# Performance work log

Hardware: AMD Instinct MI355X
Metric: run time of the kernel (lower is better)

The kernel has to match this reference:

```python
import jax, jax.numpy as jnp
import numpy as np

B, T, DM, H, DH = 4, 2048, 1024, 16, 64
DI = H * DH
CLIP = 1.0
LN_EPS = 1e-5


def setup_inputs() -> dict:
    key = jax.random.key(0)
    ks = jax.random.split(key, 9)

    def xav(k, shape):  # xavier_uniform, fan_in=shape[1], fan_out=shape[0]
        lim = float(np.sqrt(6.0 / (shape[0] + shape[1])))
        return jax.random.uniform(k, shape, jnp.float32, -lim, lim)

    def kai(k, shape):  # default nn.Linear weight init
        lim = float(1.0 / np.sqrt(shape[1]))
        return jax.random.uniform(k, shape, jnp.float32, -lim, lim)

    return {
        "x": jax.random.normal(ks[0], (B, T, DM), jnp.float32),
        "Wq": xav(ks[1], (DI, DM)),
        "Wk": xav(ks[2], (DI, DM)),
        "Wv": xav(ks[3], (DI, DM)),
        "Wa": kai(ks[4], (DI, DM)), "ba": jnp.full((DI,), 3.0, jnp.float32),
        "Wb": kai(ks[5], (H, DM)), "bb": jnp.zeros((H,), jnp.float32),
        "Wg": kai(ks[6], (H, DM)), "bg": jnp.zeros((H,), jnp.float32),
        "WaR": kai(ks[7], (DI, DM)), "baR": jnp.full((DI,), 3.0, jnp.float32),
        "Wo": xav(ks[8], (DM, DI)),
        "ln_w": jnp.ones((DM,), jnp.float32),
        "ln_b": jnp.zeros((DM,), jnp.float32),
    }


def reference(x, Wq, Wk, Wv, Wa, ba, Wb, bb, Wg, bg, WaR, baR, Wo, ln_w, ln_b):
    Bs, Ts, _ = x.shape
    residual = x
    # LayerNorm
    mu = jnp.mean(x, -1, keepdims=True)
    var = jnp.mean((x - mu) ** 2, -1, keepdims=True)
    xn = (x - mu) / jnp.sqrt(var + LN_EPS) * ln_w + ln_b

    q = (xn @ Wq.T).reshape(Bs, Ts, H, DH)
    k = (xn @ Wk.T).reshape(Bs, Ts, H, DH)
    v = (xn @ Wv.T).reshape(Bs, Ts, H, DH)
    alpha = jax.nn.sigmoid(xn @ Wa.T + ba).reshape(Bs, Ts, H, DH)
    aR = jax.nn.sigmoid(xn @ WaR.T + baR).reshape(Bs, Ts, H, DH)
    beta = jax.nn.sigmoid(xn @ Wb.T + bb)   # (B,T,H)
    gamma = jax.nn.sigmoid(xn @ Wg.T + bg)  # (B,T,H)

    tm = lambda a: jnp.moveaxis(a, 1, 0)  # time-major for scan
    xs = (tm(q), tm(k), tm(v), tm(alpha), tm(aR), tm(beta), tm(gamma))
    S0 = jnp.zeros((Bs, H, DH, DH), x.dtype)

    def step(carry, inp):
        S, R = carry
        q_t, k_t, v_t, a_t, aR_t, b_t, g_t = inp  # (B,H,d) / (B,H)
        kn = k_t / jnp.maximum(jnp.linalg.norm(k_t, axis=-1, keepdims=True), 1e-12)
        # residual target from previous state: r = clip(v - S^T k)
        pred = jnp.einsum('bhji,bhj->bhi', S, kn)
        r = jnp.clip(v_t - pred, -CLIP, CLIP)
        # primary state: S = diag(alpha) S; S += beta k (v - k^T S)
        S = a_t[..., None] * S
        kp = jnp.einsum('bhd,bhde->bhe', kn, S)
        S = S + b_t[..., None, None] * kn[..., None] * (v_t - kp)[..., None, :]
        o = jnp.einsum('bhji,bhj->bhi', S, q_t)
        # residual state
        R = aR_t[..., None] * R
        kpR = jnp.einsum('bhd,bhde->bhe', kn, R)
        R = R + g_t[..., None, None] * kn[..., None] * (r - kpR)[..., None, :]
        o = o + jnp.einsum('bhji,bhj->bhi', R, q_t)
        return (S, R), o

    _, os = jax.lax.scan(step, (S0, S0), xs)  # os: (T,B,H,d)
    out = jnp.moveaxis(os, 0, 1).reshape(Bs, Ts, DI) @ Wo.T
    return out + residual  # dropout is identity at inference
```

## Files before the change

kernel.cpp:

```cpp
#include <hip/hip_runtime.h>
#include <hip/hip_fp16.h>

#define B_SZ 4
#define T_SEQ 2048
#define NH 16
#define HD 64
#define DMODEL 1024
#define MTOT (B_SZ * T_SEQ)

typedef __bf16 bf16x8 __attribute__((ext_vector_type(8)));
typedef float f32x4 __attribute__((ext_vector_type(4)));
typedef float f32x2 __attribute__((ext_vector_type(2)));
typedef _Float16 f16x4 __attribute__((ext_vector_type(4)));

__device__ __forceinline__ unsigned short f2bf(float f) {
    union { float f; unsigned int i; } c; c.f = f;
    unsigned int u = c.i;
    u += 0x7fffu + ((u >> 16) & 1u);
    return (unsigned short)(u >> 16);
}
__device__ __forceinline__ float sigm(float x) { return 1.f / (1.f + __expf(-x)); }

__device__ __forceinline__ void dma16(const void* g, void* l) {
    __builtin_amdgcn_global_load_lds(
        (const __attribute__((address_space(1))) void*)g,
        (__attribute__((address_space(3))) void*)l, 16, 0, 0);
}

template <int CTRL>
__device__ __forceinline__ float dppadd(float x) {
    int v = __builtin_amdgcn_update_dpp(0, __builtin_bit_cast(int, x), CTRL, 0xf, 0xf, false);
    return x + __builtin_bit_cast(float, v);
}
__device__ __forceinline__ float rowsum16(float x) {
    x = dppadd<0x128>(x);
    x = dppadd<0x124>(x);
    x = dppadd<0x122>(x);
    x = dppadd<0x121>(x);
    return x;
}

__device__ __forceinline__ void rowsum3(float& a, float& b, float& c) {
    a = rowsum16(a);
    b = rowsum16(b);
    c = rowsum16(c);
}

__global__ __launch_bounds__(256, 1) void k_ln(const float* __restrict__ x,
                                               const float* __restrict__ lnw,
                                               const float* __restrict__ lnb,
                                               unsigned short* __restrict__ xn) {
    const int m = blockIdx.x;
    const int t = threadIdx.x;
    float4 xv = ((const float4*)(x + (size_t)m * DMODEL))[t];
    float s = xv.x + xv.y + xv.z + xv.w;
    float s2 = xv.x * xv.x + xv.y * xv.y + xv.z * xv.z + xv.w * xv.w;
#pragma unroll
    for (int off = 32; off >= 1; off >>= 1) {
        s += __shfl_xor(s, off);
        s2 += __shfl_xor(s2, off);
    }
    __shared__ float red[8];
    const int wid = t >> 6;
    if ((t & 63) == 0) { red[wid] = s; red[4 + wid] = s2; }
    __syncthreads();
    if (t == 0) {
        float su = red[0] + red[1] + red[2] + red[3];
        float sq = red[4] + red[5] + red[6] + red[7];
        float mu = su * (1.f / DMODEL);
        float var = sq * (1.f / DMODEL) - mu * mu;
        red[0] = mu;
        red[1] = rsqrtf(var + 1e-5f);
    }
    __syncthreads();
    float mu = red[0], rstd = red[1];
    float4 w4 = ((const float4*)lnw)[t];
    float4 b4 = ((const float4*)lnb)[t];
    ushort4 o;
    o.x = f2bf((xv.x - mu) * rstd * w4.x + b4.x);
    o.y = f2bf((xv.y - mu) * rstd * w4.y + b4.y);
    o.z = f2bf((xv.z - mu) * rstd * w4.z + b4.z);
    o.w = f2bf((xv.w - mu) * rstd * w4.w + b4.w);
    ((ushort4*)(xn + (size_t)m * DMODEL))[t] = o;
}

struct WPtrs { const float* p0; const float* p1; const float* p2; const float* p3; const float* p4; };

__global__ __launch_bounds__(256, 1) void k_wconv(WPtrs w, unsigned short* __restrict__ dst) {
    const int plane = blockIdx.y;
    const float* src = plane == 0 ? w.p0 : plane == 1 ? w.p1 : plane == 2 ? w.p2
                                                             : plane == 3 ? w.p3 : w.p4;
    const size_t i = ((size_t)blockIdx.x * 256 + threadIdx.x) * 8;
    float4 f0 = *(const float4*)(src + i);
    float4 f1 = *(const float4*)(src + i + 4);
    uint4 o;
    o.x = (unsigned)f2bf(f0.x) | ((unsigned)f2bf(f0.y) << 16);
    o.y = (unsigned)f2bf(f0.z) | ((unsigned)f2bf(f0.w) << 16);
    o.z = (unsigned)f2bf(f1.x) | ((unsigned)f2bf(f1.y) << 16);
    o.w = (unsigned)f2bf(f1.z) | ((unsigned)f2bf(f1.w) << 16);
    *(uint4*)(dst + (size_t)plane * 1048576 + i) = o;
}

__global__ __launch_bounds__(256, 1) void k_cvt1(const float* __restrict__ src,
                                                 unsigned short* __restrict__ dst) {
    const size_t i = ((size_t)blockIdx.x * 256 + threadIdx.x) * 8;
    float4 f0 = *(const float4*)(src + i);
    float4 f1 = *(const float4*)(src + i + 4);
    uint4 o;
    o.x = (unsigned)f2bf(f0.x) | ((unsigned)f2bf(f0.y) << 16);
    o.y = (unsigned)f2bf(f0.z) | ((unsigned)f2bf(f0.w) << 16);
    o.z = (unsigned)f2bf(f1.x) | ((unsigned)f2bf(f1.y) << 16);
    o.w = (unsigned)f2bf(f1.z) | ((unsigned)f2bf(f1.w) << 16);
    *(uint4*)(dst + i) = o;
}

template <int KDIM>
__device__ __forceinline__ void gemm128(const unsigned short* __restrict__ A,
                                        const unsigned short* __restrict__ Bw,
                                        int m0, int n0, f32x4 acc[4][4]) {
    __shared__ __align__(16) unsigned short sA[128 * 32];
    __shared__ __align__(16) unsigned short sB[128 * 32];

    const int t = threadIdx.x;
    const int lane = t & 63;
    const int wv = t >> 6;
    const int wm = wv >> 1, wn = wv & 1;
    const int ml = lane & 15, kq = lane >> 4;

#pragma unroll
    for (int i = 0; i < 4; i++)
#pragma unroll
        for (int j = 0; j < 4; j++) {
            f32x4 z; z[0] = 0.f; z[1] = 0.f; z[2] = 0.f; z[3] = 0.f;
            acc[i][j] = z;
        }

    const unsigned short* pA = A + (size_t)m0 * KDIM;
    const unsigned short* pB = Bw + (size_t)n0 * KDIM;
    const unsigned short* gA0 = pA + (size_t)(t >> 2) * KDIM + (t & 3) * 8;
    const unsigned short* gA1 = gA0 + (size_t)64 * KDIM;
    const unsigned short* gB0 = pB + (size_t)(t >> 2) * KDIM + (t & 3) * 8;
    const unsigned short* gB1 = gB0 + (size_t)64 * KDIM;
    unsigned short* lA0 = sA + wv * 512;
    unsigned short* lA1 = lA0 + 2048;
    unsigned short* lB0 = sB + wv * 512;
    unsigned short* lB1 = lB0 + 2048;

    for (int kb = 0; kb < KDIM / 32; kb++) {
        const int ko = kb * 32;
        dma16(gA0 + ko, lA0);
        dma16(gA1 + ko, lA1);
        dma16(gB0 + ko, lB0);
        dma16(gB1 + ko, lB1);
        __syncthreads();
        bf16x8 af[4], bfr[4];
#pragma unroll
        for (int mt = 0; mt < 4; mt++)
            af[mt] = *(const bf16x8*)&sA[(wm * 64 + mt * 16 + ml) * 32 + kq * 8];
#pragma unroll
        for (int nt = 0; nt < 4; nt++)
            bfr[nt] = *(const bf16x8*)&sB[(wn * 64 + nt * 16 + ml) * 32 + kq * 8];
#pragma unroll
        for (int mt = 0; mt < 4; mt++)
#pragma unroll
            for (int nt = 0; nt < 4; nt++)
                acc[mt][nt] = __builtin_amdgcn_mfma_f32_16x16x32_bf16(af[mt], bfr[nt], acc[mt][nt], 0, 0, 0);
        __syncthreads();
    }
}

template <typename OT>
__global__ __launch_bounds__(256, 1) void k_proj(const unsigned short* __restrict__ xn,
                                                 const unsigned short* __restrict__ wbf,
                                                 const float* __restrict__ ba,
                                                 const float* __restrict__ baR,
                                                 OT* __restrict__ qo, OT* __restrict__ ko,
                                                 OT* __restrict__ vo, OT* __restrict__ ao,
                                                 OT* __restrict__ aRo) {
    const int m0 = blockIdx.x * 128;
    const int yt = blockIdx.y;
    const int widx = yt >> 3;
    const int n0 = (yt & 7) * 128;
    const unsigned short* W = wbf + (size_t)widx * 1048576;
    f32x4 acc[4][4];
    gemm128<1024>(xn, W, m0, n0, acc);

    OT* outp = widx == 0 ? qo : widx == 1 ? ko : widx == 2 ? vo : widx == 3 ? ao : aRo;
    const float* bias = (widx == 3) ? ba : (widx == 4) ? baR : (const float*)0;
    const int lane = threadIdx.x & 63;
    const int wv = threadIdx.x >> 6;
    const int wm = wv >> 1, wn = wv & 1;
    const int ml = lane & 15, kq = lane >> 4;
#pragma unroll
    for (int mt = 0; mt < 4; mt++)
#pragma unroll
        for (int nt = 0; nt < 4; nt++) {
            const int rowg = m0 + wm * 64 + mt * 16 + kq * 4;
            const int colg = n0 + wn * 64 + nt * 16 + ml;
            float bval = bias ? bias[colg] : 0.f;
#pragma unroll
            for (int r = 0; r < 4; r++) {
                float v = acc[mt][nt][r];
                if (widx >= 3) v = sigm(v + bval);
                outp[(size_t)(rowg + r) * DMODEL + colg] = (OT)v;
            }
        }
}

__global__ __launch_bounds__(256, 1) void k_bg(const unsigned short* __restrict__ xn,
                                               const float* __restrict__ Wb,
                                               const float* __restrict__ bb,
                                               const float* __restrict__ Wg,
                                               const float* __restrict__ bgp,
                                               f32x2* __restrict__ bgpk) {
    const int m = blockIdx.x;
    const int t = threadIdx.x;
    const int h = t >> 4, seg = t & 15;
    const ushort4* xr = (const ushort4*)(xn + (size_t)m * DMODEL + seg * 64);
    const float4* wbr = (const float4*)(Wb + (size_t)h * DMODEL + seg * 64);
    const float4* wgr = (const float4*)(Wg + (size_t)h * DMODEL + seg * 64);
    float db = 0.f, dg = 0.f;
#pragma unroll
    for (int u = 0; u < 16; u++) {
        ushort4 a = xr[u];
        float4 w1 = wbr[u], w2 = wgr[u];
        union { unsigned int i; float f; } c0, c1, c2, c3;
        c0.i = ((unsigned int)a.x) << 16; c1.i = ((unsigned int)a.y) << 16;
        c2.i = ((unsigned int)a.z) << 16; c3.i = ((unsigned int)a.w) << 16;
        db += c0.f * w1.x + c1.f * w1.y + c2.f * w1.z + c3.f * w1.w;
        dg += c0.f * w2.x + c1.f * w2.y + c2.f * w2.z + c3.f * w2.w;
    }
#pragma unroll
    for (int off = 1; off < 16; off <<= 1) {
        db += __shfl_xor(db, off);
        dg += __shfl_xor(dg, off);
    }
    if (seg == 0) {
        f32x2 o;
        o[0] = sigm(db + bb[h]);
        o[1] = sigm(dg + bgp[h]);
        bgpk[(size_t)m * NH + h] = o;
    }
}

__global__ __launch_bounds__(256, 1) void k_prep16(__half* __restrict__ kb) {
    const int row = blockIdx.x * 16 + (threadIdx.x >> 4);
    const int tr = threadIdx.x & 15;
    const int bh = row >> 11, t = row & 2047;
    const size_t idx = ((size_t)((bh >> 4) * T_SEQ + t)) * DMODEL + (bh & 15) * 64 + tr * 4;
    f16x4 k4 = *(const f16x4*)((const __half*)kb + idx);
    float k0 = (float)k4[0], k1 = (float)k4[1], k2 = (float)k4[2], k3 = (float)k4[3];
    float ss = k0 * k0 + k1 * k1 + k2 * k2 + k3 * k3;
    ss = rowsum16(ss);
    float inv = 1.f / fmaxf(sqrtf(ss), 1e-12f);
    f16x4 o;
    o[0] = (_Float16)(k0 * inv); o[1] = (_Float16)(k1 * inv);
    o[2] = (_Float16)(k2 * inv); o[3] = (_Float16)(k3 * inv);
    *(f16x4*)(kb + idx) = o;
}

__global__ __launch_bounds__(256, 1) void k_prep32(float* __restrict__ kb) {
    const int row = blockIdx.x * 16 + (threadIdx.x >> 4);
    const int tr = threadIdx.x & 15;
    const int bh = row >> 11, t = row & 2047;
    const size_t idx = ((size_t)((bh >> 4) * T_SEQ + t)) * DMODEL + (bh & 15) * 64 + tr * 4;
    f32x4 k4 = *(const f32x4*)(kb + idx);
    float ss = k4[0] * k4[0] + k4[1] * k4[1] + k4[2] * k4[2] + k4[3] * k4[3];
    ss = rowsum16(ss);
    float inv = 1.f / fmaxf(sqrtf(ss), 1e-12f);
    f32x4 o;
    o[0] = k4[0] * inv; o[1] = k4[1] * inv; o[2] = k4[2] * inv; o[3] = k4[3] * inv;
    *(f32x4*)(kb + idx) = o;
}

__global__ __launch_bounds__(256, 1) void k_scan32(const float* __restrict__ qb,
                                                   const float* __restrict__ knb,
                                                   const float* __restrict__ vb,
                                                   const float* __restrict__ ab,
                                                   const float* __restrict__ aRb,
                                                   const f32x2* __restrict__ bgpk,
                                                   unsigned short* __restrict__ ob) {
    const int blk = blockIdx.x;
    const int bh = blk & 63, cg = blk >> 6;
    const int b = bh >> 4, h = bh & 15;
    const int t = threadIdx.x;
    const int col = t >> 4, tr = t & 15;
    const int ii = cg * 16 + col;
    const int j0 = tr * 4;

    const size_t blkoff = (size_t)b * T_SEQ * DMODEL + h * 64;
    const float* pq = qb + blkoff;
    const float* pk = knb + blkoff;
    const float* pa = ab + blkoff;
    const float* pr = aRb + blkoff;
    const float* pvb = vb + blkoff;
    const f32x2* pbg = bgpk + (size_t)b * T_SEQ * NH + h;
    unsigned short* obp = ob + blkoff + ii;

    f32x2 S01 = {0.f, 0.f}, S23 = {0.f, 0.f}, R01 = {0.f, 0.f}, R23 = {0.f, 0.f};

    f32x4 rk[6], rq[6], ra[6], rr[6];
    float rv[6];
    f32x2 rbg[6];

#pragma unroll
    for (int p = 0; p < 6; p++) {
        const size_t vo = (size_t)p * DMODEL;
        rk[p] = *(const f32x4*)(pk + vo + j0);
        rq[p] = *(const f32x4*)(pq + vo + j0);
        ra[p] = *(const f32x4*)(pa + vo + j0);
        rr[p] = *(const f32x4*)(pr + vo + j0);
        rv[p] = pvb[vo + ii];
        rbg[p] = pbg[(size_t)p * NH];
    }

    float oA, oB, oC;

#define SCAN_BODY32(P, ODEST)                                                       \
    {                                                                               \
        const f32x2 kn01 = {rk[P][0], rk[P][1]}, kn23 = {rk[P][2], rk[P][3]};       \
        const f32x2 a01 = {ra[P][0], ra[P][1]}, a23 = {ra[P][2], ra[P][3]};         \
        const f32x2 x01 = {rr[P][0], rr[P][1]}, x23 = {rr[P][2], rr[P][3]};         \
        const f32x2 q01 = {rq[P][0], rq[P][1]}, q23 = {rq[P][2], rq[P][3]};         \
        const float vc = rv[P];                                                     \
        const float beta = rbg[P][0], gamma = rbg[P][1];                            \
        const f32x2 Sd01 = a01 * S01, Sd23 = a23 * S23;                             \
        const f32x2 Rd01 = x01 * R01, Rd23 = x23 * R23;                             \
        const f32x2 pv2 = S01 * kn01 + S23 * kn23;                                  \
        const f32x2 kp2 = Sd01 * kn01 + Sd23 * kn23;                                \
        const f32x2 kR2 = Rd01 * kn01 + Rd23 * kn23;                                \
        float pred = pv2[0] + pv2[1];                                               \
        float kp = kp2[0] + kp2[1];                                                 \
        float kpR = kR2[0] + kR2[1];                                                \
        rowsum3(pred, kp, kpR);                                                     \
        const float rres = fminf(fmaxf(vc - pred, -1.f), 1.f);                      \
        const float cS = beta * (vc - kp);                                          \
        const float cR = gamma * (rres - kpR);                                      \
        const f32x2 cS2 = {cS, cS}, cR2 = {cR, cR};                                 \
        S01 = cS2 * kn01 + Sd01; S23 = cS2 * kn23 + Sd23;                           \
        R01 = cR2 * kn01 + Rd01; R23 = cR2 * kn23 + Rd23;                           \
        const f32x2 ov = (S01 + R01) * q01 + (S23 + R23) * q23;                     \
        ODEST = ov[0] + ov[1];                                                      \
              \
        {                                                                           \
            const int sp = (st + (P) + 6) & (T_SEQ - 1);                            \
            const size_t vo = (size_t)sp * DMODEL;                                  \
            rk[P] = *(const f32x4*)(pk + vo + j0);                                  \
            rq[P] = *(const f32x4*)(pq + vo + j0);                                  \
            ra[P] = *(const f32x4*)(pa + vo + j0);                                  \
            rr[P] = *(const f32x4*)(pr + vo + j0);                                  \
            rv[P] = pvb[vo + ii];                                                   \
            rbg[P] = pbg[(size_t)sp * NH];                                          \
        }                                                                           \
    }

#define FLUSH3(SBASE)                                                               \
    {                                                                               \
        rowsum3(oA, oB, oC);                                                        \
        if (tr == 0) {                                                              \
            if ((SBASE) < T_SEQ)     obp[(size_t)(SBASE) * DMODEL] = f2bf(oA);      \
            if ((SBASE) + 1 < T_SEQ) obp[(size_t)((SBASE) + 1) * DMODEL] = f2bf(oB);\
            if ((SBASE) + 2 < T_SEQ) obp[(size_t)((SBASE) + 2) * DMODEL] = f2bf(oC);\
        }                                                                           \
    }

    for (int st = 0; st < T_SEQ; st += 6) {
        SCAN_BODY32(0, oA)
        SCAN_BODY32(1, oB)
        SCAN_BODY32(2, oC)
        FLUSH3(st)
        SCAN_BODY32(3, oA)
        SCAN_BODY32(4, oB)
        SCAN_BODY32(5, oC)
        FLUSH3(st + 3)
    }
#undef SCAN_BODY32
#undef FLUSH3
}

__global__ __launch_bounds__(256, 1) void k_scan16(const __half* __restrict__ qb,
                                                   const __half* __restrict__ knb,
                                                   const __half* __restrict__ vb,
                                                   const __half* __restrict__ ab,
                                                   const __half* __restrict__ aRb,
                                                   const f32x2* __restrict__ bgpk,
                                                   unsigned short* __restrict__ ob) {
    const int blk = blockIdx.x;
    const int bh = blk & 63, cg = blk >> 6;
    const int b = bh >> 4, h = bh & 15;
    const int t = threadIdx.x;
    const int col = t >> 4, tr = t & 15;
    const int ii = cg * 16 + col;
    const int j0 = tr * 4;

    const size_t vecbase = ((size_t)b * T_SEQ) * DMODEL + h * 64 + j0;
    const size_t vbase = ((size_t)b * T_SEQ) * DMODEL + h * 64 + ii;
    const size_t bgbase = ((size_t)b * T_SEQ) * NH + h;

    const __half* pk = knb + vecbase;
    const __half* pq = qb + vecbase;
    const __half* pa = ab + vecbase;
    const __half* pr = aRb + vecbase;

    float S0 = 0, S1 = 0, S2 = 0, S3 = 0, R0 = 0, R1 = 0, R2 = 0, R3 = 0;

    f16x4 rk[6], rq[6], ra[6], rr[6];
    __half rv[6];
    f32x2 rbg[6];
    f32x4 fkn[6], fq[6], fa[6], fr[6];
    float fv[6];

#pragma unroll
    for (int p = 0; p < 6; p++) {
        const size_t voff = (size_t)p * DMODEL;
        rk[p] = *(const f16x4*)(pk + voff);
        rq[p] = *(const f16x4*)(pq + voff);
        ra[p] = *(const f16x4*)(pa + voff);
        rr[p] = *(const f16x4*)(pr + voff);
        rv[p] = vb[vbase + voff];
        rbg[p] = bgpk[bgbase + (size_t)p * NH];
    }
    fkn[0][0] = (float)rk[0][0]; fkn[0][1] = (float)rk[0][1]; fkn[0][2] = (float)rk[0][2]; fkn[0][3] = (float)rk[0][3];
    fq[0][0] = (float)rq[0][0]; fq[0][1] = (float)rq[0][1]; fq[0][2] = (float)rq[0][2]; fq[0][3] = (float)rq[0][3];
    fa[0][0] = (float)ra[0][0]; fa[0][1] = (float)ra[0][1]; fa[0][2] = (float)ra[0][2]; fa[0][3] = (float)ra[0][3];
    fr[0][0] = (float)rr[0][0]; fr[0][1] = (float)rr[0][1]; fr[0][2] = (float)rr[0][2]; fr[0][3] = (float)rr[0][3];
    fv[0] = (float)rv[0];

#define SCAN_BODY(P, PN)                                                              \
    {                                                                                 \
        const int s = st + (P);                                                       \
        const float beta = rbg[P][0], gamma = rbg[P][1];                              \
        {                                                                             \
            const size_t voff = (size_t)((s + 6) & (T_SEQ - 1)) * DMODEL;             \
            rk[P] = *(const f16x4*)(pk + voff);                                       \
            rq[P] = *(const f16x4*)(pq + voff);                                       \
            ra[P] = *(const f16x4*)(pa + voff);                                       \
            rr[P] = *(const f16x4*)(pr + voff);                                       \
            rv[P] = vb[vbase + voff];                                                 \
        }                                                                             \
        fkn[PN][0] = (float)rk[PN][0]; fkn[PN][1] = (float)rk[PN][1];                 \
        fkn[PN][2] = (float)rk[PN][2]; fkn[PN][3] = (float)rk[PN][3];                 \
        fq[PN][0] = (float)rq[PN][0]; fq[PN][1] = (float)rq[PN][1];                   \
        fq[PN][2] = (float)rq[PN][2]; fq[PN][3] = (float)rq[PN][3];                   \
        fa[PN][0] = (float)ra[PN][0]; fa[PN][1] = (float)ra[PN][1];                   \
        fa[PN][2] = (float)ra[PN][2]; fa[PN][3] = (float)ra[PN][3];                   \
        fr[PN][0] = (float)rr[PN][0]; fr[PN][1] = (float)rr[PN][1];                   \
        fr[PN][2] = (float)rr[PN][2]; fr[PN][3] = (float)rr[PN][3];                   \
        fv[PN] = (float)rv[PN];                                                       \
        {                                                                             \
            const float kn0 = fkn[P][0], kn1 = fkn[P][1], kn2 = fkn[P][2], kn3 = fkn[P][3]; \
            const float a0 = fa[P][0], a1 = fa[P][1], a2 = fa[P][2], a3 = fa[P][3];   \
            const float x0 = fr[P][0], x1 = fr[P][1], x2 = fr[P][2], x3 = fr[P][3];   \
            const float vc = fv[P];                                                   \
            float pred = S0 * kn0 + S1 * kn1 + S2 * kn2 + S3 * kn3;                   \
            float Sd0 = a0 * S0, Sd1 = a1 * S1, Sd2 = a2 * S2, Sd3 = a3 * S3;         \
            float Rd0 = x0 * R0, Rd1 = x1 * R1, Rd2 = x2 * R2, Rd3 = x3 * R3;         \
            float kp = Sd0 * kn0 + Sd1 * kn1 + Sd2 * kn2 + Sd3 * kn3;                 \
            float kpR = Rd0 * kn0 + Rd1 * kn1 + Rd2 * kn2 + Rd3 * kn3;                \
            pred = rowsum16(pred);                                                    \
            kp = rowsum16(kp);                                                        \
            kpR = rowsum16(kpR);                                                      \
            const float rres = fminf(fmaxf(vc - pred, -1.f), 1.f);                    \
            const float cS = beta * (vc - kp);                                        \
            const float cR = gamma * (rres - kpR);                                    \
            S0 = fmaf(cS, kn0, Sd0); S1 = fmaf(cS, kn1, Sd1);                         \
            S2 = fmaf(cS, kn2, Sd2); S3 = fmaf(cS, kn3, Sd3);                         \
            R0 = fmaf(cR, kn0, Rd0); R1 = fmaf(cR, kn1, Rd1);                         \
            R2 = fmaf(cR, kn2, Rd2); R3 = fmaf(cR, kn3, Rd3);                         \
            float o = (S0 + R0) * fq[P][0] + (S1 + R1) * fq[P][1] +                   \
                      (S2 + R2) * fq[P][2] + (S3 + R3) * fq[P][3];                    \
            o = rowsum16(o);                                                          \
            if (tr == 0 && s < T_SEQ)                                                 \
                ob[vbase + (size_t)s * DMODEL] = f2bf(o);                             \
        }                                                                             \
        rbg[P] = bgpk[bgbase + (size_t)((s + 6) & (T_SEQ - 1)) * NH];                 \
    }

    for (int st = 0; st < T_SEQ; st += 6) {
        SCAN_BODY(0, 1)
        SCAN_BODY(1, 2)
        SCAN_BODY(2, 3)
        SCAN_BODY(3, 4)
        SCAN_BODY(4, 5)
        SCAN_BODY(5, 0)
    }
#undef SCAN_BODY
}

__global__ __launch_bounds__(256, 1) void k_out(const unsigned short* __restrict__ ob,
                                                const unsigned short* __restrict__ wobf,
                                                const float* __restrict__ x,
                                                float* __restrict__ out) {
    const int m0 = blockIdx.x * 128;
    const int n0 = blockIdx.y * 128;
    f32x4 acc[4][4];
    gemm128<1024>(ob, wobf, m0, n0, acc);
    const int lane = threadIdx.x & 63;
    const int wv = threadIdx.x >> 6;
    const int wm = wv >> 1, wn = wv & 1;
    const int ml = lane & 15, kq = lane >> 4;
#pragma unroll
    for (int mt = 0; mt < 4; mt++)
#pragma unroll
        for (int nt = 0; nt < 4; nt++) {
            const int rowg = m0 + wm * 64 + mt * 16 + kq * 4;
            const int colg = n0 + wn * 64 + nt * 16 + ml;
#pragma unroll
            for (int r = 0; r < 4; r++) {
                size_t idx = (size_t)(rowg + r) * DMODEL + colg;
                out[idx] = acc[mt][nt][r] + x[idx];
            }
        }
}

extern "C" void kernel_launch(void* const* d_in, const int* in_sizes, int n_in,
                              void* d_out, int out_size, void* d_ws, size_t ws_size,
                              hipStream_t stream) {
    const float* x = (const float*)d_in[0];
    const float* Wq = (const float*)d_in[1];
    const float* Wk = (const float*)d_in[2];
    const float* Wv = (const float*)d_in[3];
    const float* Wa = (const float*)d_in[4];
    const float* ba = (const float*)d_in[5];
    const float* Wb = (const float*)d_in[6];
    const float* bb = (const float*)d_in[7];
    const float* Wg = (const float*)d_in[8];
    const float* bg = (const float*)d_in[9];
    const float* WaR = (const float*)d_in[10];
    const float* baR = (const float*)d_in[11];
    const float* Wo = (const float*)d_in[12];
    const float* lnw = (const float*)d_in[13];
    const float* lnb = (const float*)d_in[14];

    const size_t SZH = 16777216ULL;
    const size_t SZF = 33554432ULL;
    const size_t need32 = 5 * SZF + SZH + 2097152ULL;
    const size_t need16 = 6 * SZH + 2097152ULL;

    char* ws = (char*)d_ws;
    unsigned short* wbf = (unsigned short*)d_out;
    WPtrs wp{Wq, Wk, Wv, Wa, WaR};

    if (ws_size >= need32) {
        float* qb = (float*)(ws + 0 * SZF);
        float* kb = (float*)(ws + 1 * SZF);
        float* vb = (float*)(ws + 2 * SZF);
        float* ab = (float*)(ws + 3 * SZF);
        float* aRb = (float*)(ws + 4 * SZF);
        unsigned short* xn = (unsigned short*)(ws + 5 * SZF);
        f32x2* bgpk = (f32x2*)(ws + 5 * SZF + SZH);
        unsigned short* wobf = (unsigned short*)qb;

        k_wconv<<<dim3(512, 5), dim3(256), 0, stream>>>(wp, wbf);
        k_ln<<<dim3(MTOT), dim3(256), 0, stream>>>(x, lnw, lnb, xn);
        k_proj<float><<<dim3(64, 40), dim3(256), 0, stream>>>(xn, wbf, ba, baR, qb, kb, vb, ab, aRb);
        k_bg<<<dim3(MTOT), dim3(256), 0, stream>>>(xn, Wb, bb, Wg, bg, bgpk);
        k_prep32<<<dim3(MTOT * NH / 16), dim3(256), 0, stream>>>(kb);
        k_scan32<<<dim3(256), dim3(256), 0, stream>>>(qb, kb, vb, ab, aRb, bgpk, xn);
        k_cvt1<<<dim3(512), dim3(256), 0, stream>>>(Wo, wobf);
        k_out<<<dim3(64, 8), dim3(256), 0, stream>>>(xn, wobf, x, (float*)d_out);
    } else if (ws_size >= need16) {
        __half* qb = (__half*)(ws + 0 * SZH);
        __half* kb = (__half*)(ws + 1 * SZH);
        __half* vb = (__half*)(ws + 2 * SZH);
        __half* ab = (__half*)(ws + 3 * SZH);
        __half* aRb = (__half*)(ws + 4 * SZH);
        unsigned short* xn = (unsigned short*)(ws + 5 * SZH);
        f32x2* bgpk = (f32x2*)(ws + 6 * SZH);
        unsigned short* wobf = (unsigned short*)qb;

        k_wconv<<<dim3(512, 5), dim3(256), 0, stream>>>(wp, wbf);
        k_ln<<<dim3(MTOT), dim3(256), 0, stream>>>(x, lnw, lnb, xn);
        k_proj<_Float16><<<dim3(64, 40), dim3(256), 0, stream>>>(
            xn, wbf, ba, baR, (_Float16*)qb, (_Float16*)kb, (_Float16*)vb, (_Float16*)ab, (_Float16*)aRb);
        k_bg<<<dim3(MTOT), dim3(256), 0, stream>>>(xn, Wb, bb, Wg, bg, bgpk);
        k_prep16<<<dim3(MTOT * NH / 16), dim3(256), 0, stream>>>(kb);
        k_scan16<<<dim3(256), dim3(256), 0, stream>>>(qb, kb, vb, ab, aRb, bgpk, xn);
        k_cvt1<<<dim3(512), dim3(256), 0, stream>>>(Wo, wobf);
        k_out<<<dim3(64, 8), dim3(256), 0, stream>>>(xn, wobf, x, (float*)d_out);
    }
}
```

Before: 835.5 us.

## Split scan state columns across 32 lanes and double scan block count

The recurrent scan kernel now gives each state column 32 lanes holding 2 elements each, instead of 16 lanes holding 4, and launches 512 blocks instead of 256 with launch bounds allowing two blocks per CU. This shortens the per-lane serial arithmetic on the critical recurrence path and raises occupancy on the latency-bound scan. The cost is an extra cross-row shuffle in every reduction and more redundant per-block loads of k, q, alpha and aR.

```diff
diff --git a/kernel.cpp b/kernel.cpp
--- a/kernel.cpp
+++ b/kernel.cpp
@@ -41,6 +41,15 @@
 }
 
 __device__ __forceinline__ void rowsum3(float& a, float& b, float& c) {
+    a = rowsum16(a);
+    b = rowsum16(b);
+    c = rowsum16(c);
+}
+
+__device__ __forceinline__ void rowsum32_3(float& a, float& b, float& c) {
+    a += __shfl_xor(a, 16);
+    b += __shfl_xor(b, 16);
+    c += __shfl_xor(c, 16);
     a = rowsum16(a);
     b = rowsum16(b);
     c = rowsum16(c);
@@ -273,7 +282,7 @@
     *(f32x4*)(kb + idx) = o;
 }
 
-__global__ __launch_bounds__(256, 1) void k_scan32(const float* __restrict__ qb,
+__global__ __launch_bounds__(256, 2) void k_scan32(const float* __restrict__ qb,
                                                    const float* __restrict__ knb,
                                                    const float* __restrict__ vb,
                                                    const float* __restrict__ ab,
@@ -284,9 +293,9 @@
     const int bh = blk & 63, cg = blk >> 6;
     const int b = bh >> 4, h = bh & 15;
     const int t = threadIdx.x;
-    const int col = t >> 4, tr = t & 15;
-    const int ii = cg * 16 + col;
-    const int j0 = tr * 4;
+    const int col = t >> 5, lr = t & 31;
+    const int ii = cg * 8 + col;
+    const int j0 = lr * 2;
 
     const size_t blkoff = (size_t)b * T_SEQ * DMODEL + h * 64;
     const float* pq = qb + blkoff;
@@ -297,19 +306,19 @@
     const f32x2* pbg = bgpk + (size_t)b * T_SEQ * NH + h;
     unsigned short* obp = ob + blkoff + ii;
 
-    f32x2 S01 = {0.f, 0.f}, S23 = {0.f, 0.f}, R01 = {0.f, 0.f}, R23 = {0.f, 0.f};
-
-    f32x4 rk[6], rq[6], ra[6], rr[6];
+    f32x2 S2 = {0.f, 0.f}, R2 = {0.f, 0.f};
+
+    f32x2 rk[6], rq[6], ra[6], rr[6];
     float rv[6];
     f32x2 rbg[6];
 
 #pragma unroll
     for (int p = 0; p < 6; p++) {
         const size_t vo = (size_t)p * DMODEL;
-        rk[p] = *(const f32x4*)(pk + vo + j0);
-        rq[p] = *(const f32x4*)(pq + vo + j0);
-        ra[p] = *(const f32x4*)(pa + vo + j0);
-        rr[p] = *(const f32x4*)(pr + vo + j0);
+        rk[p] = *(const f32x2*)(pk + vo + j0);
+        rq[p] = *(const f32x2*)(pq + vo + j0);
+        ra[p] = *(const f32x2*)(pa + vo + j0);
+        rr[p] = *(const f32x2*)(pr + vo + j0);
         rv[p] = pvb[vo + ii];
         rbg[p] = pbg[(size_t)p * NH];
     }
@@ -318,37 +327,34 @@
 
 #define SCAN_BODY32(P, ODEST)                                                       \
     {                                                                               \
-        const f32x2 kn01 = {rk[P][0], rk[P][1]}, kn23 = {rk[P][2], rk[P][3]};       \
-        const f32x2 a01 = {ra[P][0], ra[P][1]}, a23 = {ra[P][2], ra[P][3]};         \
-        const f32x2 x01 = {rr[P][0], rr[P][1]}, x23 = {rr[P][2], rr[P][3]};         \
-        const f32x2 q01 = {rq[P][0], rq[P][1]}, q23 = {rq[P][2], rq[P][3]};         \
+        const f32x2 kn2 = rk[P], a2 = ra[P], x2 = rr[P], q2 = rq[P];                \
         const float vc = rv[P];                                                     \
         const float beta = rbg[P][0], gamma = rbg[P][1];                            \
-        const f32x2 Sd01 = a01 * S01, Sd23 = a23 * S23;                             \
-        const f32x2 Rd01 = x01 * R01, Rd23 = x23 * R23;                             \
-        const f32x2 pv2 = S01 * kn01 + S23 * kn23;                                  \
-        const f32x2 kp2 = Sd01 * kn01 + Sd23 * kn23;                                \
-        const f32x2 kR2 = Rd01 * kn01 + Rd23 * kn23;                                \
-        float pred = pv2[0] + pv2[1];                                               \
-        float kp = kp2[0] + kp2[1];                                                 \
+        const f32x2 Sd = a2 * S2;                                                   \
+        const f32x2 Rd = x2 * R2;                                                   \
+        const f32x2 pp = S2 * kn2;                                                  \
+        const f32x2 kq2 = Sd * kn2;                                                 \
+        const f32x2 kR2 = Rd * kn2;                                                 \
+        float pred = pp[0] + pp[1];                                                 \
+        float kp = kq2[0] + kq2[1];                                                 \
         float kpR = kR2[0] + kR2[1];                                                \
-        rowsum3(pred, kp, kpR);                                                     \
+        rowsum32_3(pred, kp, kpR);                                                  \
         const float rres = fminf(fmaxf(vc - pred, -1.f), 1.f);                      \
         const float cS = beta * (vc - kp);                                          \
         const float cR = gamma * (rres - kpR);                                      \
         const f32x2 cS2 = {cS, cS}, cR2 = {cR, cR};                                 \
-        S01 = cS2 * kn01 + Sd01; S23 = cS2 * kn23 + Sd23;                           \
-        R01 = cR2 * kn01 + Rd01; R23 = cR2 * kn23 + Rd23;                           \
-        const f32x2 ov = (S01 + R01) * q01 + (S23 + R23) * q23;                     \
+        S2 = cS2 * kn2 + Sd;                                                        \
+        R2 = cR2 * kn2 + Rd;                                                        \
+        const f32x2 ov = (S2 + R2) * q2;                                            \
         ODEST = ov[0] + ov[1];                                                      \
               \
         {                                                                           \
             const int sp = (st + (P) + 6) & (T_SEQ - 1);                            \
             const size_t vo = (size_t)sp * DMODEL;                                  \
-            rk[P] = *(const f32x4*)(pk + vo + j0);                                  \
-            rq[P] = *(const f32x4*)(pq + vo + j0);                                  \
-            ra[P] = *(const f32x4*)(pa + vo + j0);                                  \
-            rr[P] = *(const f32x4*)(pr + vo + j0);                                  \
+            rk[P] = *(const f32x2*)(pk + vo + j0);                                  \
+            rq[P] = *(const f32x2*)(pq + vo + j0);                                  \
+            ra[P] = *(const f32x2*)(pa + vo + j0);                                  \
+            rr[P] = *(const f32x2*)(pr + vo + j0);                                  \
             rv[P] = pvb[vo + ii];                                                   \
             rbg[P] = pbg[(size_t)sp * NH];                                          \
         }                                                                           \
@@ -356,8 +362,8 @@
 
 #define FLUSH3(SBASE)                                                               \
     {                                                                               \
-        rowsum3(oA, oB, oC);                                                        \
-        if (tr == 0) {                                                              \
+        rowsum32_3(oA, oB, oC);                                                     \
+        if (lr == 0) {                                                              \
             if ((SBASE) < T_SEQ)     obp[(size_t)(SBASE) * DMODEL] = f2bf(oA);      \
             if ((SBASE) + 1 < T_SEQ) obp[(size_t)((SBASE) + 1) * DMODEL] = f2bf(oB);\
             if ((SBASE) + 2 < T_SEQ) obp[(size_t)((SBASE) + 2) * DMODEL] = f2bf(oC);\
@@ -556,7 +562,7 @@
         k_proj<float><<<dim3(64, 40), dim3(256), 0, stream>>>(xn, wbf, ba, baR, qb, kb, vb, ab, aRb);
         k_bg<<<dim3(MTOT), dim3(256), 0, stream>>>(xn, Wb, bb, Wg, bg, bgpk);
         k_prep32<<<dim3(MTOT * NH / 16), dim3(256), 0, stream>>>(kb);
-        k_scan32<<<dim3(256), dim3(256), 0, stream>>>(qb, kb, vb, ab, aRb, bgpk, xn);
+        k_scan32<<<dim3(512), dim3(256), 0, stream>>>(qb, kb, vb, ab, aRb, bgpk, xn);
         k_cvt1<<<dim3(512), dim3(256), 0, stream>>>(Wo, wobf);
         k_out<<<dim3(64, 8), dim3(256), 0, stream>>>(xn, wobf, x, (float*)d_out);
     } else if (ws_size >= need16) {
```

Result: slower. 1.181 ms (+41.4%).
